# Performance work log

Hardware: AMD Instinct MI355X
Metric: run time of the kernel (lower is better)

Reference implementation:

```python
import jax, jax.numpy as jnp
import numpy as np

N_NODES = 50000
N_EDGES = 500000
D_IN = 128
D_OUT = 128
NUM_GRAPHS = 512


def sage_conv(x, src, dst, W_l, W_r, num_nodes):
    # mean aggregation of source-node features onto target nodes
    msg = x[src]  # [E, D]
    agg = jax.ops.segment_sum(msg, dst, num_segments=num_nodes)
    cnt = jax.ops.segment_sum(jnp.ones((src.shape[0], 1), x.dtype), dst,
                              num_segments=num_nodes)
    agg = agg / jnp.maximum(cnt, 1.0)
    # PyG SAGEConv (bias=False): lin_l(agg) + lin_r(x); torch Linear is x @ W.T
    return agg @ W_l.T + x @ W_r.T


def setup_inputs() -> dict:
    key = jax.random.key(0)
    ks = jax.random.split(key, 7)
    x = jax.random.normal(ks[0], (N_NODES, D_IN), dtype=jnp.float32)
    edge_index = jax.random.randint(ks[1], (2, N_EDGES), 0, N_NODES, dtype=jnp.int64)
    batch = jnp.sort(jax.random.randint(ks[2], (N_NODES,), 0, NUM_GRAPHS, dtype=jnp.int64))
    s = 1.0 / np.sqrt(D_IN)
    W_l1 = jax.random.uniform(ks[3], (D_OUT, D_IN), jnp.float32, -s, s)
    W_r1 = jax.random.uniform(ks[4], (D_OUT, D_IN), jnp.float32, -s, s)
    W_l2 = jax.random.uniform(ks[5], (D_OUT, D_OUT), jnp.float32, -s, s)
    W_r2 = jax.random.uniform(ks[6], (D_OUT, D_OUT), jnp.float32, -s, s)
    return {"x": x, "edge_index": edge_index, "batch": batch,
            "W_l1": W_l1, "W_r1": W_r1, "W_l2": W_l2, "W_r2": W_r2}


def reference(x, edge_index, batch, W_l1, W_r1, W_l2, W_r2):
    src, dst = edge_index[0], edge_index[1]
    # dropout p=0.0 -> identity
    x1 = jax.nn.relu(sage_conv(x, src, dst, W_l1, W_r1, N_NODES))
    x2 = jax.nn.relu(sage_conv(x1, src, dst, W_l2, W_r2, N_NODES))
    xs = jnp.concatenate([x1, x2], axis=-1)  # JumpingKnowledge('cat')
    pooled = jax.ops.segment_max(xs, batch, num_segments=NUM_GRAPHS)
    # guard empty graphs (segment_max yields -inf there)
    return jnp.where(jnp.isfinite(pooled), pooled, 0.0)
```

## Files before the change

### kernel.cpp

```cpp
#include <hip/hip_runtime.h>
#include <hip/hip_bf16.h>

#define N_NODES 50000
#define N_EDGES 500000
#define D 128
#define NUM_GRAPHS 512
#define BM 128
#define NB_NODES 196
#define CVT_HALF 3125
#define OUT_BLOCKS 128
#define WC_BLOCKS 16

typedef __attribute__((ext_vector_type(8))) short bf16x8;
typedef __attribute__((ext_vector_type(4))) float f32x4;

static __device__ __forceinline__ unsigned short f2b(float f) {
  __hip_bfloat16 h = __float2bfloat16(f);
  return *reinterpret_cast<unsigned short*>(&h);
}
static __device__ __forceinline__ float blo(unsigned int p) {
  return __uint_as_float(p << 16);
}
static __device__ __forceinline__ float bhi(unsigned int p) {
  return __uint_as_float(p & 0xffff0000u);
}

static __device__ __forceinline__ void cvt_chunk(
    const float* __restrict__ x, unsigned short* __restrict__ xb, int blk) {
  int i = (blk * 256 + (int)threadIdx.x) * 4;
  if (i < N_NODES * D) {
    float4 f = *(const float4*)&x[i];
    ushort4 o = make_ushort4(f2b(f.x), f2b(f.y), f2b(f.z), f2b(f.w));
    *(ushort4*)&xb[i] = o;
  }
}


__global__ __launch_bounds__(256) void k_prep(
    const float* __restrict__ x, unsigned short* __restrict__ xb,
    int* __restrict__ deg, float* __restrict__ out,
    const float* __restrict__ Wl1, const float* __restrict__ Wr1,
    const float* __restrict__ Wl2, const float* __restrict__ Wr2,
    unsigned short* __restrict__ wc1, unsigned short* __restrict__ wc2) {
  int b = blockIdx.x;
  if (b < NB_NODES) {
    int i = b * 256 + threadIdx.x;
    if (i < N_NODES) deg[i] = 0;
  } else if (b < NB_NODES + OUT_BLOCKS) {
    int i = ((b - NB_NODES) * 256 + threadIdx.x) * 4;
    if (i < NUM_GRAPHS * 2 * D)
      *(float4*)&out[i] = make_float4(0.f, 0.f, 0.f, 0.f);
  } else {
    int b2 = b - NB_NODES - OUT_BLOCKS;
    int layer = b2 >> 4;
    int idx = (b2 & 15) * 256 + threadIdx.x;
    int j = idx >> 5;
    int kg = idx & 31;
    int k0 = kg * 8;
    const float* wl = layer ? Wl2 : Wl1;
    const float* wr = layer ? Wr2 : Wr1;
    const float* srcp = (k0 < D) ? (wl + j * D + k0) : (wr + j * D + (k0 - D));
    float4 f0 = *(const float4*)srcp;
    float4 f1 = *(const float4*)(srcp + 4);
    bf16x8 wv;
    wv[0] = (short)f2b(f0.x); wv[1] = (short)f2b(f0.y);
    wv[2] = (short)f2b(f0.z); wv[3] = (short)f2b(f0.w);
    wv[4] = (short)f2b(f1.x); wv[5] = (short)f2b(f1.y);
    wv[6] = (short)f2b(f1.z); wv[7] = (short)f2b(f1.w);
    unsigned short* wc = layer ? wc2 : wc1;
    int byteofs = j * 512 + ((kg * 16) ^ ((j & 7) << 4));
    *(bf16x8*)((char*)wc + byteofs) = wv;
  }
}


__global__ void k_count(const int* __restrict__ dst, int* __restrict__ deg) {
  int e = blockIdx.x * 256 + threadIdx.x;
  if (e < N_EDGES) atomicAdd(&deg[dst[e]], 1);
}

__global__ __launch_bounds__(256) void k_scanA(
    const int* __restrict__ deg, int* __restrict__ bsum, int* __restrict__ pos,
    const float* __restrict__ x, unsigned short* __restrict__ xb) {
  int b = blockIdx.x;
  if (b >= NB_NODES) { cvt_chunk(x, xb, b - NB_NODES); return; }
  __shared__ int s[256];
  int t = threadIdx.x;
  int i = b * 256 + t;
  int v = (i < N_NODES) ? deg[i] : 0;
  s[t] = v;
  __syncthreads();
  for (int off = 1; off < 256; off <<= 1) {
    int add = (t >= off) ? s[t - off] : 0;
    __syncthreads();
    s[t] += add;
    __syncthreads();
  }
  if (i < N_NODES) pos[i] = s[t] - v;
  if (t == 255) bsum[b] = s[255];
}

__global__ __launch_bounds__(256) void k_scanB(
    const int* __restrict__ deg, const int* __restrict__ bsum,
    int* __restrict__ rowptr, int* __restrict__ pos,
    const float* __restrict__ x, unsigned short* __restrict__ xb) {
  int b = blockIdx.x;
  if (b >= NB_NODES) { cvt_chunk(x, xb, CVT_HALF + b - NB_NODES); return; }
  __shared__ int s[256];
  int t = threadIdx.x;
  s[t] = (t < b) ? bsum[t] : 0;
  __syncthreads();
  for (int off = 128; off > 0; off >>= 1) {
    if (t < off) s[t] += s[t + off];
    __syncthreads();
  }
  int offset = s[0];
  int i = b * 256 + t;
  if (i < N_NODES) {
    int excl = pos[i] + offset;
    rowptr[i] = excl;
    pos[i] = excl;
    if (i == N_NODES - 1) rowptr[N_NODES] = excl + deg[i];
  }
}

__global__ void k_bucket(const int* __restrict__ src, const int* __restrict__ dst,
                         int* __restrict__ pos, int* __restrict__ esrc) {
  int e = blockIdx.x * 256 + threadIdx.x;
  if (e < N_EDGES) {
    int slot = atomicAdd(&pos[dst[e]], 1);
    esrc[slot] = src[e];
  }
}


__global__ __launch_bounds__(256) void k_agg(
    const unsigned short* __restrict__ xb, const int* __restrict__ rowptr,
    const int* __restrict__ esrc, unsigned short* __restrict__ aggb) {
  int node = (blockIdx.x * 256 + threadIdx.x) >> 6;
  int lane = threadIdx.x & 63;
  if (node >= N_NODES) return;
  const int q = lane >> 4;
  const int c = lane & 15;
  int beg = rowptr[node], end = rowptr[node + 1];

  float acc[8];
#pragma unroll
  for (int i = 0; i < 8; ++i) acc[i] = 0.f;

  int e = beg + q;
  for (; e + 4 < end; e += 8) {
    int s0 = esrc[e];
    int s1 = esrc[e + 4];
    uint4 p0 = *(const uint4*)&xb[(size_t)s0 * D + c * 8];
    uint4 p1 = *(const uint4*)&xb[(size_t)s1 * D + c * 8];
    acc[0] += blo(p0.x) + blo(p1.x); acc[1] += bhi(p0.x) + bhi(p1.x);
    acc[2] += blo(p0.y) + blo(p1.y); acc[3] += bhi(p0.y) + bhi(p1.y);
    acc[4] += blo(p0.z) + blo(p1.z); acc[5] += bhi(p0.z) + bhi(p1.z);
    acc[6] += blo(p0.w) + blo(p1.w); acc[7] += bhi(p0.w) + bhi(p1.w);
  }
  if (e < end) {
    int s0 = esrc[e];
    uint4 p = *(const uint4*)&xb[(size_t)s0 * D + c * 8];
    acc[0] += blo(p.x); acc[1] += bhi(p.x);
    acc[2] += blo(p.y); acc[3] += bhi(p.y);
    acc[4] += blo(p.z); acc[5] += bhi(p.z);
    acc[6] += blo(p.w); acc[7] += bhi(p.w);
  }

#pragma unroll
  for (int i = 0; i < 8; ++i) {
    acc[i] += __shfl_xor(acc[i], 16);
    acc[i] += __shfl_xor(acc[i], 32);
  }

  if (q == 0) {
    float inv = 1.f / fmaxf((float)(end - beg), 1.f);
    uint4 o;
    o.x = (unsigned int)f2b(acc[0] * inv) | ((unsigned int)f2b(acc[1] * inv) << 16);
    o.y = (unsigned int)f2b(acc[2] * inv) | ((unsigned int)f2b(acc[3] * inv) << 16);
    o.z = (unsigned int)f2b(acc[4] * inv) | ((unsigned int)f2b(acc[5] * inv) << 16);
    o.w = (unsigned int)f2b(acc[6] * inv) | ((unsigned int)f2b(acc[7] * inv) << 16);
    *(uint4*)&aggb[(size_t)node * D + c * 8] = o;
  }
}


__global__ __launch_bounds__(512) void k_gemm(
    const unsigned short* __restrict__ Ab, const unsigned short* __restrict__ Xb,
    const unsigned short* __restrict__ Wc,
    unsigned short* __restrict__ Yb, const int* __restrict__ batch,
    unsigned int* __restrict__ pool, int col_ofs) {
  __shared__ unsigned short Wlds[32768 + 256];
  const int tid = threadIdx.x;
  const int w = tid >> 6, lane = tid & 63;
  const int lr = lane & 15, lh = lane >> 4;
  const int row0 = blockIdx.x * BM;
  const int row = row0 + w * 16 + lr;

#pragma unroll
  for (int i = 0; i < 8; ++i) {
    int ofs = i * 8192 + tid * 16;
    *(bf16x8*)((char*)Wlds + ofs) = *(const bf16x8*)((const char*)Wc + ofs);
  }

  bf16x8 a[8];
  if (row < N_NODES) {
    const unsigned short* ar = Ab + (size_t)row * D;
    const unsigned short* xr = Xb + (size_t)row * D;
#pragma unroll
    for (int kk = 0; kk < 4; ++kk)
      a[kk] = *(const bf16x8*)(ar + kk * 32 + lh * 8);
#pragma unroll
    for (int kk = 0; kk < 4; ++kk)
      a[4 + kk] = *(const bf16x8*)(xr + kk * 32 + lh * 8);
  } else {
#pragma unroll
    for (int kk = 0; kk < 8; ++kk)
      a[kk] = (bf16x8){0, 0, 0, 0, 0, 0, 0, 0};
  }
  __syncthreads();

  f32x4 acc[8];
#pragma unroll
  for (int jt = 0; jt < 8; ++jt) acc[jt] = (f32x4){0.f, 0.f, 0.f, 0.f};

#pragma unroll
  for (int jt = 0; jt < 8; ++jt) {
    int jj = jt * 16 + lr;
    const char* wbase = (const char*)Wlds + jj * 512;
    int sw = (jj & 7) << 4;
#pragma unroll
    for (int kk = 0; kk < 8; ++kk) {
      bf16x8 b = *(const bf16x8*)(wbase + ((kk * 64 + lh * 16) ^ sw));
      acc[jt] = __builtin_amdgcn_mfma_f32_16x16x32_bf16(a[kk], b, acc[jt], 0, 0, 0);
    }
  }

  __syncthreads();
#pragma unroll
  for (int jt = 0; jt < 8; ++jt) {
#pragma unroll
    for (int r = 0; r < 4; ++r) {
      int rl = w * 16 + lh * 4 + r;
      int col = jt * 16 + lr;
      float v = acc[jt][r];
      v = v > 0.f ? v : 0.f;
      int byteofs = rl * 256 + ((col * 2) ^ ((rl & 7) << 4));
      *(unsigned short*)((char*)Wlds + byteofs) = f2b(v);
    }
  }
  int* sb = (int*)(Wlds + 32768);
  if (tid < BM) {
    int grow = row0 + tid;
    sb[tid] = (grow < N_NODES) ? batch[grow] : -1;
  }
  __syncthreads();

  if (Yb != nullptr) {
    int rl = tid >> 2, c0 = (tid & 3) * 64;
    int grow = row0 + rl;
    if (grow < N_NODES) {
#pragma unroll
      for (int cc = 0; cc < 4; ++cc) {
        int byteofs = rl * 256 + ((c0 + cc * 16) ^ ((rl & 7) << 4));
        bf16x8 v = *(const bf16x8*)((char*)Wlds + byteofs);
        *(bf16x8*)&Yb[(size_t)grow * D + (c0 + cc * 16) / 2] = v;
      }
    }
  }

  {
    int col = tid & 127;
    int r0 = (tid >> 7) * 32;
    unsigned short run = 0;
    int curg = sb[r0];
    for (int r = r0; r < r0 + 32; ++r) {
      int g = sb[r];
      if (g != curg) {
        if (curg >= 0 && run)
          atomicMax(&pool[curg * (2 * D) + col_ofs + col], ((unsigned int)run) << 16);
        curg = g;
        run = 0;
      }
      int byteofs = r * 256 + ((col * 2) ^ ((r & 7) << 4));
      unsigned short v = *(const unsigned short*)((char*)Wlds + byteofs);
      run = run > v ? run : v;
    }
    if (curg >= 0 && run)
      atomicMax(&pool[curg * (2 * D) + col_ofs + col], ((unsigned int)run) << 16);
  }
}


extern "C" void kernel_launch(void* const* d_in, const int* in_sizes, int n_in,
                              void* d_out, int out_size, void* d_ws, size_t ws_size,
                              hipStream_t stream) {
  const float* x = (const float*)d_in[0];
  const int* ei = (const int*)d_in[1];
  const int* src = ei;
  const int* dst = ei + N_EDGES;
  const int* batch = (const int*)d_in[2];
  const float* Wl1 = (const float*)d_in[3];
  const float* Wr1 = (const float*)d_in[4];
  const float* Wl2 = (const float*)d_in[5];
  const float* Wr2 = (const float*)d_in[6];

  char* ws = (char*)d_ws;
  size_t off = 0;
  auto alloc = [&](size_t bytes) -> void* {
    void* p = ws + off;
    off += (bytes + 511) & ~(size_t)511;
    return p;
  };
  int* deg = (int*)alloc((size_t)N_NODES * 4);
  int* rowptr = (int*)alloc((size_t)(N_NODES + 1) * 4);
  int* pos = (int*)alloc((size_t)N_NODES * 4);
  int* bsum = (int*)alloc(256 * 4);
  int* esrc = (int*)alloc((size_t)N_EDGES * 4);
  unsigned short* xb = (unsigned short*)alloc((size_t)N_NODES * D * 2);
  unsigned short* aggb = (unsigned short*)alloc((size_t)N_NODES * D * 2);
  unsigned short* x1b = (unsigned short*)alloc((size_t)N_NODES * D * 2);
  unsigned short* wc1 = (unsigned short*)alloc(65536);
  unsigned short* wc2 = (unsigned short*)alloc(65536);
  (void)ws_size; (void)in_sizes; (void)n_in; (void)out_size;

  k_prep<<<NB_NODES + OUT_BLOCKS + 2 * WC_BLOCKS, 256, 0, stream>>>(
      x, xb, deg, (float*)d_out, Wl1, Wr1, Wl2, Wr2, wc1, wc2);

  k_count<<<(N_EDGES + 255) / 256, 256, 0, stream>>>(dst, deg);
  k_scanA<<<NB_NODES + CVT_HALF, 256, 0, stream>>>(deg, bsum, pos, x, xb);
  k_scanB<<<NB_NODES + CVT_HALF, 256, 0, stream>>>(deg, bsum, rowptr, pos, x, xb);
  k_bucket<<<(N_EDGES + 255) / 256, 256, 0, stream>>>(src, dst, pos, esrc);

  int agg_blocks = (N_NODES * 64 + 255) / 256;
  int gemm_blocks = (N_NODES + BM - 1) / BM;

  k_agg<<<agg_blocks, 256, 0, stream>>>(xb, rowptr, esrc, aggb);
  k_gemm<<<gemm_blocks, 512, 0, stream>>>(aggb, xb, wc1, x1b, batch,
                                          (unsigned int*)d_out, 0);
  k_agg<<<agg_blocks, 256, 0, stream>>>(x1b, rowptr, esrc, aggb);
  k_gemm<<<gemm_blocks, 512, 0, stream>>>(aggb, x1b, wc2, nullptr, batch,
                                          (unsigned int*)d_out, D);
}
```

Before: 139.7 us.

## Fuse mean aggregation into the SAGE GEMM kernel, dropping the agg buffer

Each GEMM block now gathers and averages neighbor features for its 128 rows itself, each wave handling 16 nodes in turn and shuffling the results into MFMA A-fragments. This removes the separate aggregation kernel, its intermediate bf16 buffer write and re-read, and two launches per forward pass. In exchange, the gather runs with far fewer concurrent waves and serialized per-node loops, which reduces the memory-level parallelism available to hide random-access latency.

```diff
diff --git a/kernel.cpp b/kernel.cpp
--- a/kernel.cpp
+++ b/kernel.cpp
@@ -134,60 +134,10 @@
 }
 
 
-__global__ __launch_bounds__(256) void k_agg(
-    const unsigned short* __restrict__ xb, const int* __restrict__ rowptr,
-    const int* __restrict__ esrc, unsigned short* __restrict__ aggb) {
-  int node = (blockIdx.x * 256 + threadIdx.x) >> 6;
-  int lane = threadIdx.x & 63;
-  if (node >= N_NODES) return;
-  const int q = lane >> 4;
-  const int c = lane & 15;
-  int beg = rowptr[node], end = rowptr[node + 1];
-
-  float acc[8];
-#pragma unroll
-  for (int i = 0; i < 8; ++i) acc[i] = 0.f;
-
-  int e = beg + q;
-  for (; e + 4 < end; e += 8) {
-    int s0 = esrc[e];
-    int s1 = esrc[e + 4];
-    uint4 p0 = *(const uint4*)&xb[(size_t)s0 * D + c * 8];
-    uint4 p1 = *(const uint4*)&xb[(size_t)s1 * D + c * 8];
-    acc[0] += blo(p0.x) + blo(p1.x); acc[1] += bhi(p0.x) + bhi(p1.x);
-    acc[2] += blo(p0.y) + blo(p1.y); acc[3] += bhi(p0.y) + bhi(p1.y);
-    acc[4] += blo(p0.z) + blo(p1.z); acc[5] += bhi(p0.z) + bhi(p1.z);
-    acc[6] += blo(p0.w) + blo(p1.w); acc[7] += bhi(p0.w) + bhi(p1.w);
-  }
-  if (e < end) {
-    int s0 = esrc[e];
-    uint4 p = *(const uint4*)&xb[(size_t)s0 * D + c * 8];
-    acc[0] += blo(p.x); acc[1] += bhi(p.x);
-    acc[2] += blo(p.y); acc[3] += bhi(p.y);
-    acc[4] += blo(p.z); acc[5] += bhi(p.z);
-    acc[6] += blo(p.w); acc[7] += bhi(p.w);
-  }
-
-#pragma unroll
-  for (int i = 0; i < 8; ++i) {
-    acc[i] += __shfl_xor(acc[i], 16);
-    acc[i] += __shfl_xor(acc[i], 32);
-  }
-
-  if (q == 0) {
-    float inv = 1.f / fmaxf((float)(end - beg), 1.f);
-    uint4 o;
-    o.x = (unsigned int)f2b(acc[0] * inv) | ((unsigned int)f2b(acc[1] * inv) << 16);
-    o.y = (unsigned int)f2b(acc[2] * inv) | ((unsigned int)f2b(acc[3] * inv) << 16);
-    o.z = (unsigned int)f2b(acc[4] * inv) | ((unsigned int)f2b(acc[5] * inv) << 16);
-    o.w = (unsigned int)f2b(acc[6] * inv) | ((unsigned int)f2b(acc[7] * inv) << 16);
-    *(uint4*)&aggb[(size_t)node * D + c * 8] = o;
-  }
-}
-
-
-__global__ __launch_bounds__(512) void k_gemm(
-    const unsigned short* __restrict__ Ab, const unsigned short* __restrict__ Xb,
+__global__ __launch_bounds__(512) void k_fused(
+    const unsigned short* __restrict__ Gs,
+    const unsigned short* __restrict__ Xb,
+    const int* __restrict__ rowptr, const int* __restrict__ esrc,
     const unsigned short* __restrict__ Wc,
     unsigned short* __restrict__ Yb, const int* __restrict__ batch,
     unsigned int* __restrict__ pool, int col_ofs) {
@@ -203,21 +153,71 @@
     int ofs = i * 8192 + tid * 16;
     *(bf16x8*)((char*)Wlds + ofs) = *(const bf16x8*)((const char*)Wc + ofs);
   }
+  int* sb = (int*)(Wlds + 32768);
+  if (tid < BM) {
+    int grow = row0 + tid;
+    sb[tid] = (grow < N_NODES) ? batch[grow] : -1;
+  }
 
   bf16x8 a[8];
+  for (int j = 0; j < 16; ++j) {
+    int node = row0 + w * 16 + j;
+    uint4 o = make_uint4(0, 0, 0, 0);
+    if (node < N_NODES) {
+      int beg = rowptr[node], end = rowptr[node + 1];
+      float acc[8];
+#pragma unroll
+      for (int i = 0; i < 8; ++i) acc[i] = 0.f;
+      int e = beg + lh;
+      for (; e + 4 < end; e += 8) {
+        int s0 = esrc[e];
+        int s1 = esrc[e + 4];
+        uint4 p0 = *(const uint4*)&Gs[(size_t)s0 * D + lr * 8];
+        uint4 p1 = *(const uint4*)&Gs[(size_t)s1 * D + lr * 8];
+        acc[0] += blo(p0.x) + blo(p1.x); acc[1] += bhi(p0.x) + bhi(p1.x);
+        acc[2] += blo(p0.y) + blo(p1.y); acc[3] += bhi(p0.y) + bhi(p1.y);
+        acc[4] += blo(p0.z) + blo(p1.z); acc[5] += bhi(p0.z) + bhi(p1.z);
+        acc[6] += blo(p0.w) + blo(p1.w); acc[7] += bhi(p0.w) + bhi(p1.w);
+      }
+      if (e < end) {
+        int s0 = esrc[e];
+        uint4 p = *(const uint4*)&Gs[(size_t)s0 * D + lr * 8];
+        acc[0] += blo(p.x); acc[1] += bhi(p.x);
+        acc[2] += blo(p.y); acc[3] += bhi(p.y);
+        acc[4] += blo(p.z); acc[5] += bhi(p.z);
+        acc[6] += blo(p.w); acc[7] += bhi(p.w);
+      }
+#pragma unroll
+      for (int i = 0; i < 8; ++i) {
+        acc[i] += __shfl_xor(acc[i], 16);
+        acc[i] += __shfl_xor(acc[i], 32);
+      }
+      float inv = 1.f / fmaxf((float)(end - beg), 1.f);
+      o.x = (unsigned int)f2b(acc[0] * inv) | ((unsigned int)f2b(acc[1] * inv) << 16);
+      o.y = (unsigned int)f2b(acc[2] * inv) | ((unsigned int)f2b(acc[3] * inv) << 16);
+      o.z = (unsigned int)f2b(acc[4] * inv) | ((unsigned int)f2b(acc[5] * inv) << 16);
+      o.w = (unsigned int)f2b(acc[6] * inv) | ((unsigned int)f2b(acc[7] * inv) << 16);
+    }
+#pragma unroll
+    for (int kk = 0; kk < 4; ++kk) {
+      int g = kk * 4 + lh;
+      uint4 t;
+      t.x = __shfl(o.x, g);
+      t.y = __shfl(o.y, g);
+      t.z = __shfl(o.z, g);
+      t.w = __shfl(o.w, g);
+      if (lr == j) a[kk] = *reinterpret_cast<bf16x8*>(&t);
+    }
+  }
   if (row < N_NODES) {
-    const unsigned short* ar = Ab + (size_t)row * D;
     const unsigned short* xr = Xb + (size_t)row * D;
-#pragma unroll
-    for (int kk = 0; kk < 4; ++kk)
-      a[kk] = *(const bf16x8*)(ar + kk * 32 + lh * 8);
 #pragma unroll
     for (int kk = 0; kk < 4; ++kk)
       a[4 + kk] = *(const bf16x8*)(xr + kk * 32 + lh * 8);
   } else {
 #pragma unroll
-    for (int kk = 0; kk < 8; ++kk)
-      a[kk] = (bf16x8){0, 0, 0, 0, 0, 0, 0, 0};
+    for (int kk = 0; kk < 4; ++kk)
+      a[4 + kk] = (bf16x8){0, 0, 0, 0, 0, 0, 0, 0};
   }
   __syncthreads();
 
@@ -249,11 +249,6 @@
       int byteofs = rl * 256 + ((col * 2) ^ ((rl & 7) << 4));
       *(unsigned short*)((char*)Wlds + byteofs) = f2b(v);
     }
-  }
-  int* sb = (int*)(Wlds + 32768);
-  if (tid < BM) {
-    int grow = row0 + tid;
-    sb[tid] = (grow < N_NODES) ? batch[grow] : -1;
   }
   __syncthreads();
 
@@ -319,7 +314,6 @@
   int* bsum = (int*)alloc(256 * 4);
   int* esrc = (int*)alloc((size_t)N_EDGES * 4);
   unsigned short* xb = (unsigned short*)alloc((size_t)N_NODES * D * 2);
-  unsigned short* aggb = (unsigned short*)alloc((size_t)N_NODES * D * 2);
   unsigned short* x1b = (unsigned short*)alloc((size_t)N_NODES * D * 2);
   unsigned short* wc1 = (unsigned short*)alloc(65536);
   unsigned short* wc2 = (unsigned short*)alloc(65536);
@@ -333,13 +327,10 @@
   k_scanB<<<NB_NODES + CVT_HALF, 256, 0, stream>>>(deg, bsum, rowptr, pos, x, xb);
   k_bucket<<<(N_EDGES + 255) / 256, 256, 0, stream>>>(src, dst, pos, esrc);
 
-  int agg_blocks = (N_NODES * 64 + 255) / 256;
   int gemm_blocks = (N_NODES + BM - 1) / BM;
 
-  k_agg<<<agg_blocks, 256, 0, stream>>>(xb, rowptr, esrc, aggb);
-  k_gemm<<<gemm_blocks, 512, 0, stream>>>(aggb, xb, wc1, x1b, batch,
-                                          (unsigned int*)d_out, 0);
-  k_agg<<<agg_blocks, 256, 0, stream>>>(x1b, rowptr, esrc, aggb);
-  k_gemm<<<gemm_blocks, 512, 0, stream>>>(aggb, x1b, wc2, nullptr, batch,
-                                          (unsigned int*)d_out, D);
-}
+  k_fused<<<gemm_blocks, 512, 0, stream>>>(xb, xb, rowptr, esrc, wc1, x1b, batch,
+                                           (unsigned int*)d_out, 0);
+  k_fused<<<gemm_blocks, 512, 0, stream>>>(x1b, x1b, rowptr, esrc, wc2, nullptr, batch,
+                                           (unsigned int*)d_out, D);
+}
```

New measurement: 167.3 us. 19.8% more time.
